# Kernel tuning notes

Measured on AMD Instinct MI355X. Metric: run time of the kernel, lower is better.

The kernel has to match this reference:

```python
import jax, jax.numpy as jnp
import numpy as np

PE_DIM = 64

def _layernorm(x, g, b, eps=1e-5):
    m = jnp.mean(x, -1, keepdims=True)
    v = jnp.mean((x - m) ** 2, -1, keepdims=True)
    return (x - m) * jax.lax.rsqrt(v + eps) * g + b

def _sinusoidal_pe(t, dim=PE_DIM):
    half = dim // 2
    freqs = jnp.exp(-jnp.log(10000.0) * jnp.arange(half) / half).astype(t.dtype)
    ang = t[..., None] * freqs  # [..., half]
    return jnp.concatenate([jnp.sin(ang), jnp.cos(ang)], -1)

def _bilinear(feats, b, t, x, y):
    # feats [B,Wl,H,W,D]; b,t int32 [B,Q,Wl,M] (b broadcastable); x,y in [0,1]
    # matches torch grid_sample(mode=bilinear, padding_mode=border, align_corners=False)
    H, W = feats.shape[2], feats.shape[3]
    px = x * W - 0.5
    py = y * H - 0.5
    x0 = jnp.floor(px); y0 = jnp.floor(py)
    wx = (px - x0)[..., None]; wy = (py - y0)[..., None]
    x0i = jnp.clip(x0.astype(jnp.int32), 0, W - 1)
    x1i = jnp.clip(x0.astype(jnp.int32) + 1, 0, W - 1)
    y0i = jnp.clip(y0.astype(jnp.int32), 0, H - 1)
    y1i = jnp.clip(y0.astype(jnp.int32) + 1, 0, H - 1)
    v00 = feats[b, t, y0i, x0i]  # [B,Q,Wl,M,D]
    v01 = feats[b, t, y0i, x1i]
    v10 = feats[b, t, y1i, x0i]
    v11 = feats[b, t, y1i, x1i]
    return (v00 * (1 - wy) * (1 - wx) + v01 * (1 - wy) * wx
            + v10 * wy * (1 - wx) + v11 * wy * wx)

def setup_inputs() -> dict:
    key = jax.random.key(0)
    ks = jax.random.split(key, 20)
    B, Q, Wl, H, W, D, M = 4, 300, 8, 64, 64, 256, 4
    s = 0.02
    inp = {
        'q': jax.random.normal(ks[0], (B, Q, D), jnp.float32),
        'kv_feats': jax.random.normal(ks[1], (B, Wl, H, W, D), jnp.float32),
        'kv_mask': jnp.zeros((B, Wl, H, W), jnp.bool_),
        'delta_sec': jax.random.normal(ks[2], (B, Q, Wl), jnp.float32),
        'w_ref': jax.random.normal(ks[3], (D, 2), jnp.float32) * s,
        'b_ref': jnp.zeros((2,), jnp.float32),
        'w_delta': jax.random.normal(ks[4], (2 * D, 3 * M), jnp.float32) * s,
        'b_delta': jnp.zeros((3 * M,), jnp.float32),
        'w_alpha': jax.random.normal(ks[5], (2 * D, M), jnp.float32) * s,
        'b_alpha': jnp.zeros((M,), jnp.float32),
        'lam': jnp.array(1.0, jnp.float32),
        'w_proj': jax.random.normal(ks[6], (D, D), jnp.float32) * s,
        'b_proj': jnp.zeros((D,), jnp.float32),
        'ln1_g': jnp.ones((D,), jnp.float32), 'ln1_b': jnp.zeros((D,), jnp.float32),
        'ln2_g': jnp.ones((D,), jnp.float32), 'ln2_b': jnp.zeros((D,), jnp.float32),
        'w_ffn1': jax.random.normal(ks[7], (D, 4 * D), jnp.float32) * s,
        'b_ffn1': jnp.zeros((4 * D,), jnp.float32),
        'w_ffn2': jax.random.normal(ks[8], (4 * D, D), jnp.float32) * s,
        'b_ffn2': jnp.zeros((D,), jnp.float32),
        'w_rel': jax.random.normal(ks[9], (PE_DIM, D), jnp.float32) * s,
        'b_rel': jnp.zeros((D,), jnp.float32),
    }
    return inp

def reference(q, kv_feats, kv_mask, delta_sec, w_ref, b_ref, w_delta, b_delta,
              w_alpha, b_alpha, lam, w_proj, b_proj, ln1_g, ln1_b, ln2_g, ln2_b,
              w_ffn1, b_ffn1, w_ffn2, b_ffn2, w_rel, b_rel):
    B, Q, D = q.shape
    Wl = kv_feats.shape[1]
    M = w_alpha.shape[1]

    qn = _layernorm(q, ln1_g, ln1_b)
    rel_feat = _sinusoidal_pe(delta_sec) @ w_rel + b_rel          # [B,Q,Wl,D]
    psi = jnp.concatenate([jnp.broadcast_to(qn[:, :, None, :], (B, Q, Wl, D)),
                           rel_feat], -1)                          # [B,Q,Wl,2D]

    delta = (psi @ w_delta + b_delta).reshape(B, Q, Wl, M, 3)
    logits = psi @ w_alpha + b_alpha                               # [B,Q,Wl,M]
    ref = jax.nn.sigmoid(qn @ w_ref + b_ref)                       # [B,Q,2]
    coords = ref[:, :, None, None, :] + jnp.tanh(delta[..., :2])   # [B,Q,Wl,M,2]
    coords = jnp.clip(coords, 0.0, 1.0)
    delta_t = jnp.tanh(delta[..., 2])                              # [B,Q,Wl,M]

    # mask features (mask==True -> invalid -> zero)
    feats = kv_feats * (~kv_mask)[..., None].astype(kv_feats.dtype)

    # temporal trilinear indices
    base = jnp.arange(Wl, dtype=q.dtype).reshape(1, 1, Wl, 1)
    target = base + delta_t
    t0f = jnp.clip(jnp.floor(target), 0, Wl - 1)
    t1f = jnp.clip(t0f + 1, 0, Wl - 1)
    alpha = (target - t0f)[..., None]
    t0 = t0f.astype(jnp.int32); t1 = t1f.astype(jnp.int32)

    bidx = jnp.arange(B, dtype=jnp.int32).reshape(B, 1, 1, 1)
    cx = coords[..., 0]; cy = coords[..., 1]
    s0 = _bilinear(feats, bidx, t0, cx, cy)                        # [B,Q,Wl,M,D]
    s1 = _bilinear(feats, bidx, t1, cx, cy)
    sampled = s0 * (1 - alpha) + s1 * alpha

    lam_sp = jax.nn.softplus(lam)
    weights = jax.nn.softmax(logits - lam_sp * jnp.abs(delta_sec)[..., None], axis=-1)
    agg = jnp.sum(weights[..., None] * sampled, axis=(2, 3))       # [B,Q,D]

    out = q + (agg @ w_proj + b_proj)
    h = _layernorm(out, ln2_g, ln2_b)
    ffn = jax.nn.gelu(h @ w_ffn1 + b_ffn1, approximate=False) @ w_ffn2 + b_ffn2
    return out + ffn
```

## Files before the change

### kernel.cpp

```cpp
#include <hip/hip_runtime.h>
#include <math.h>

#define Bn 4
#define Qn 300
#define WL 8
#define Hh 64
#define Ww 64
#define Dd 256
#define Mm 4

__device__ __forceinline__ float wave_reduce(float v) {
#pragma unroll
    for (int off = 32; off > 0; off >>= 1) v += __shfl_down(v, off, 64);
    return v;
}

__device__ __forceinline__ float block_reduce256(float v, float* lds) {
    v = wave_reduce(v);
    int lane = threadIdx.x & 63, wv = threadIdx.x >> 6;
    if (lane == 0) lds[wv] = v;
    __syncthreads();
    float r = lds[0] + lds[1] + lds[2] + lds[3];
    __syncthreads();
    return r;
}

__global__ void __launch_bounds__(256) k_pts(const float* __restrict__ q,
                                             const float* __restrict__ g1,
                                             const float* __restrict__ b1,
                                             const float* __restrict__ w_ref,
                                             const float* __restrict__ b_ref,
                                             const float* __restrict__ dsec,
                                             const float* __restrict__ w_rel,
                                             const float* __restrict__ b_rel,
                                             const float* __restrict__ w_delta,
                                             const float* __restrict__ b_delta,
                                             const float* __restrict__ w_alpha,
                                             const float* __restrict__ b_alpha,
                                             float* __restrict__ prm) {
    __shared__ float lds[4];
    __shared__ float sref[2];
    __shared__ float sqn[256];
    __shared__ float pe[8][64];
    __shared__ float rel[8][260];
    __shared__ float WcT[16 * 516];
    __shared__ float res[8][16];

    int bq = blockIdx.x, t = threadIdx.x;

    float x = q[bq * Dd + t];
    float m = block_reduce256(x, lds) * (1.f / Dd);
    float dx = x - m;
    float v = block_reduce256(dx * dx, lds) * (1.f / Dd);
    float y = dx * rsqrtf(v + 1e-5f) * g1[t] + b1[t];
    sqn[t] = y;

    float s0 = block_reduce256(y * w_ref[t * 2 + 0], lds);
    float s1 = block_reduce256(y * w_ref[t * 2 + 1], lds);
    if (t == 0) {
        sref[0] = 1.f / (1.f + expf(-(s0 + b_ref[0])));
        sref[1] = 1.f / (1.f + expf(-(s1 + b_ref[1])));
    }

    {
        int wl = t >> 5, i = t & 31;
        float f = expf(-logf(10000.f) * (float)i * (1.f / 32.f));
        float a = dsec[bq * WL + wl] * f;
        pe[wl][i] = sinf(a);
        pe[wl][i + 32] = cosf(a);
    }

    for (int u = t; u < 512 * 16; u += 256) {
        int k = u >> 4, jj = u & 15;
        float w = (jj < 12) ? w_delta[k * 12 + jj] : w_alpha[k * 4 + (jj - 12)];
        WcT[jj * 516 + k] = w;
    }

    float wr[64];
#pragma unroll
    for (int k = 0; k < 64; k++) wr[k] = w_rel[k * Dd + t];
    __syncthreads();

    float brl = b_rel[t];
    for (int wl = 0; wl < WL; wl++) {
        float r = brl;
#pragma unroll
        for (int k = 0; k < 64; k++) r += pe[wl][k] * wr[k];
        rel[wl][t] = r;
    }
    __syncthreads();

    if (t < 128) {
        int wl = t >> 4, jj = t & 15;
        const float4* wrow = (const float4*)&WcT[jj * 516];
        const float4* qrow = (const float4*)sqn;
        const float4* rrow = (const float4*)&rel[wl][0];
        float s = 0.f;
#pragma unroll 8
        for (int k4 = 0; k4 < 64; k4++) {
            float4 a = qrow[k4], w = wrow[k4];
            s += a.x * w.x + a.y * w.y + a.z * w.z + a.w * w.w;
        }
#pragma unroll 8
        for (int k4 = 0; k4 < 64; k4++) {
            float4 a = rrow[k4], w = wrow[64 + k4];
            s += a.x * w.x + a.y * w.y + a.z * w.z + a.w * w.w;
        }
        s += (jj < 12) ? b_delta[jj] : b_alpha[jj - 12];
        res[wl][jj] = s;
    }
    __syncthreads();

    if (t < 32) {
        int wl = t >> 2, mm = t & 3;
        float l0 = res[wl][12], l1 = res[wl][13], l2 = res[wl][14], l3 = res[wl][15];
        float mx = fmaxf(fmaxf(l0, l1), fmaxf(l2, l3));
        float inv = 1.f / (expf(l0 - mx) + expf(l1 - mx) + expf(l2 - mx) + expf(l3 - mx));
        float wgt = expf(res[wl][12 + mm] - mx) * inv;

        float cx = fminf(fmaxf(sref[0] + tanhf(res[wl][mm * 3 + 0]), 0.f), 1.f);
        float cy = fminf(fmaxf(sref[1] + tanhf(res[wl][mm * 3 + 1]), 0.f), 1.f);
        float tgt = (float)wl + tanhf(res[wl][mm * 3 + 2]);
        float t0f = fminf(fmaxf(floorf(tgt), 0.f), (float)(WL - 1));
        float t1f = fminf(t0f + 1.f, (float)(WL - 1));
        float alpha = tgt - t0f;
        float px = cx * (float)Ww - 0.5f, py = cy * (float)Hh - 0.5f;
        float fx = floorf(px), fy = floorf(py);
        float wx = px - fx, wy = py - fy;
        float x0 = fminf(fmaxf(fx, 0.f), (float)(Ww - 1));
        float x1 = fminf(fmaxf(fx + 1.f, 0.f), (float)(Ww - 1));
        float y0 = fminf(fmaxf(fy, 0.f), (float)(Hh - 1));
        float y1 = fminf(fmaxf(fy + 1.f, 0.f), (float)(Hh - 1));
        float* o = prm + (size_t)(bq * 32 + t) * 12;
        o[0] = wgt; o[1] = alpha; o[2] = wx; o[3] = wy;
        o[4] = t0f; o[5] = t1f; o[6] = x0; o[7] = x1; o[8] = y0; o[9] = y1;
        o[10] = 0.f; o[11] = 0.f;
    }
}

__global__ void __launch_bounds__(256) k_sample(const float* __restrict__ feats,
                                                const unsigned char* __restrict__ mask,
                                                const float* __restrict__ prm,
                                                float* __restrict__ agg) {
    __shared__ float P[32 * 12];
    __shared__ float part[4][256];
    int bq = blockIdx.x, t = threadIdx.x;
    int b = bq / Qn;
    int l = t & 63, j = t >> 6;
    for (int i = t; i < 32 * 12; i += 256) P[i] = prm[(size_t)bq * (32 * 12) + i];
    __syncthreads();
    const float4* f4 = (const float4*)feats;
    float4 acc = {0.f, 0.f, 0.f, 0.f};
#pragma unroll 2
    for (int p8 = 0; p8 < 8; p8++) {
        const float* pp = &P[(j * 8 + p8) * 12];
        float wgt = pp[0], alpha = pp[1], wx = pp[2], wy = pp[3];
        int t0 = (int)pp[4], t1 = (int)pp[5];
        int x0 = (int)pp[6], x1 = (int)pp[7];
        int y0 = (int)pp[8], y1 = (int)pp[9];
        float w00 = (1.f - wy) * (1.f - wx), w01 = (1.f - wy) * wx;
        float w10 = wy * (1.f - wx), w11 = wy * wx;
        float wt0 = wgt * (1.f - alpha), wt1 = wgt * alpha;
#pragma unroll
        for (int s = 0; s < 2; s++) {
            int tt = s ? t1 : t0;
            float wts = s ? wt1 : wt0;
            int base = (b * WL + tt) * Hh;
            int i00 = (base + y0) * Ww + x0;
            int i01 = (base + y0) * Ww + x1;
            int i10 = (base + y1) * Ww + x0;
            int i11 = (base + y1) * Ww + x1;
            float c00 = wts * w00 * (mask[i00] ? 0.f : 1.f);
            float c01 = wts * w01 * (mask[i01] ? 0.f : 1.f);
            float c10 = wts * w10 * (mask[i10] ? 0.f : 1.f);
            float c11 = wts * w11 * (mask[i11] ? 0.f : 1.f);
            float4 v00 = f4[(size_t)i00 * 64 + l];
            float4 v01 = f4[(size_t)i01 * 64 + l];
            float4 v10 = f4[(size_t)i10 * 64 + l];
            float4 v11 = f4[(size_t)i11 * 64 + l];
            acc.x += c00 * v00.x + c01 * v01.x + c10 * v10.x + c11 * v11.x;
            acc.y += c00 * v00.y + c01 * v01.y + c10 * v10.y + c11 * v11.y;
            acc.z += c00 * v00.z + c01 * v01.z + c10 * v10.z + c11 * v11.z;
            acc.w += c00 * v00.w + c01 * v01.w + c10 * v10.w + c11 * v11.w;
        }
    }
    ((float4*)&part[j][0])[l] = acc;
    __syncthreads();
    agg[(size_t)bq * Dd + t] = part[0][t] + part[1][t] + part[2][t] + part[3][t];
}

__global__ void __launch_bounds__(1024) k_out(const float* __restrict__ q,
                                              const float* __restrict__ agg,
                                              const float* __restrict__ w_proj,
                                              const float* __restrict__ b_proj,
                                              const float* __restrict__ g2,
                                              const float* __restrict__ b2,
                                              const float* __restrict__ w_ffn1,
                                              const float* __restrict__ b_ffn1,
                                              const float* __restrict__ w_ffn2,
                                              const float* __restrict__ b_ffn2,
                                              float* __restrict__ out) {
    __shared__ float sA[4][256];
    __shared__ float sO[4][256];
    __shared__ float sH[4][256];
    __shared__ float sF[4][1024];
    __shared__ float sP[4][4][256];
    __shared__ float red[4][4];
    int t = threadIdx.x;
    int c = t & 255, j = t >> 8;
    int row0 = blockIdx.x * 4;

    sA[j][c] = agg[(size_t)(row0 + j) * Dd + c];
    __syncthreads();

    {
        float a0 = 0, a1 = 0, a2 = 0, a3 = 0;
        const float4* ar0 = (const float4*)&sA[0][j * 64];
        const float4* ar1 = (const float4*)&sA[1][j * 64];
        const float4* ar2 = (const float4*)&sA[2][j * 64];
        const float4* ar3 = (const float4*)&sA[3][j * 64];
        for (int k4 = 0; k4 < 16; k4++) {
            int k = j * 64 + k4 * 4;
            float w0 = w_proj[(k + 0) * Dd + c];
            float w1 = w_proj[(k + 1) * Dd + c];
            float w2 = w_proj[(k + 2) * Dd + c];
            float w3 = w_proj[(k + 3) * Dd + c];
            float4 h0 = ar0[k4], h1 = ar1[k4], h2 = ar2[k4], h3 = ar3[k4];
            a0 += h0.x * w0 + h0.y * w1 + h0.z * w2 + h0.w * w3;
            a1 += h1.x * w0 + h1.y * w1 + h1.z * w2 + h1.w * w3;
            a2 += h2.x * w0 + h2.y * w1 + h2.z * w2 + h2.w * w3;
            a3 += h3.x * w0 + h3.y * w1 + h3.z * w2 + h3.w * w3;
        }
        sP[j][0][c] = a0; sP[j][1][c] = a1; sP[j][2][c] = a2; sP[j][3][c] = a3;
    }
    __syncthreads();

    float o = sP[0][j][c] + sP[1][j][c] + sP[2][j][c] + sP[3][j][c]
            + q[(size_t)(row0 + j) * Dd + c] + b_proj[c];
    sO[j][c] = o;
    int wg = (t >> 6) & 3, lane = t & 63;
    float s = wave_reduce(o);
    if (lane == 0) red[j][wg] = s;
    __syncthreads();
    float mean = (red[j][0] + red[j][1] + red[j][2] + red[j][3]) * (1.f / 256.f);
    float dx = o - mean;
    float s2 = wave_reduce(dx * dx);
    __syncthreads();
    if (lane == 0) red[j][wg] = s2;
    __syncthreads();
    float var = (red[j][0] + red[j][1] + red[j][2] + red[j][3]) * (1.f / 256.f);
    float h = dx * rsqrtf(var + 1e-5f) * g2[c] + b2[c];
    sH[j][c] = h;
    __syncthreads();

    {
        float f0 = 0, f1 = 0, f2 = 0, f3 = 0;
        const float4* h0p = (const float4*)&sH[0][0];
        const float4* h1p = (const float4*)&sH[1][0];
        const float4* h2p = (const float4*)&sH[2][0];
        const float4* h3p = (const float4*)&sH[3][0];
        for (int k4 = 0; k4 < 64; k4++) {
            int k = k4 * 4;
            float w0 = w_ffn1[(size_t)(k + 0) * 1024 + t];
            float w1 = w_ffn1[(size_t)(k + 1) * 1024 + t];
            float w2 = w_ffn1[(size_t)(k + 2) * 1024 + t];
            float w3 = w_ffn1[(size_t)(k + 3) * 1024 + t];
            float4 h0 = h0p[k4], h1 = h1p[k4], h2 = h2p[k4], h3 = h3p[k4];
            f0 += h0.x * w0 + h0.y * w1 + h0.z * w2 + h0.w * w3;
            f1 += h1.x * w0 + h1.y * w1 + h1.z * w2 + h1.w * w3;
            f2 += h2.x * w0 + h2.y * w1 + h2.z * w2 + h2.w * w3;
            f3 += h3.x * w0 + h3.y * w1 + h3.z * w2 + h3.w * w3;
        }
        float bf = b_ffn1[t];
        float v0 = f0 + bf, v1 = f1 + bf, v2 = f2 + bf, v3 = f3 + bf;
        sF[0][t] = 0.5f * v0 * (1.f + erff(v0 * 0.70710678118654752f));
        sF[1][t] = 0.5f * v1 * (1.f + erff(v1 * 0.70710678118654752f));
        sF[2][t] = 0.5f * v2 * (1.f + erff(v2 * 0.70710678118654752f));
        sF[3][t] = 0.5f * v3 * (1.f + erff(v3 * 0.70710678118654752f));
    }
    __syncthreads();

    {
        float a0 = 0, a1 = 0, a2 = 0, a3 = 0;
        const float4* f0p = (const float4*)&sF[0][j * 256];
        const float4* f1p = (const float4*)&sF[1][j * 256];
        const float4* f2p = (const float4*)&sF[2][j * 256];
        const float4* f3p = (const float4*)&sF[3][j * 256];
        for (int k4 = 0; k4 < 64; k4++) {
            int k = j * 256 + k4 * 4;
            float w0 = w_ffn2[(size_t)(k + 0) * Dd + c];
            float w1 = w_ffn2[(size_t)(k + 1) * Dd + c];
            float w2 = w_ffn2[(size_t)(k + 2) * Dd + c];
            float w3 = w_ffn2[(size_t)(k + 3) * Dd + c];
            float4 h0 = f0p[k4], h1 = f1p[k4], h2 = f2p[k4], h3 = f3p[k4];
            a0 += h0.x * w0 + h0.y * w1 + h0.z * w2 + h0.w * w3;
            a1 += h1.x * w0 + h1.y * w1 + h1.z * w2 + h1.w * w3;
            a2 += h2.x * w0 + h2.y * w1 + h2.z * w2 + h2.w * w3;
            a3 += h3.x * w0 + h3.y * w1 + h3.z * w2 + h3.w * w3;
        }
        sP[j][0][c] = a0; sP[j][1][c] = a1; sP[j][2][c] = a2; sP[j][3][c] = a3;
    }
    __syncthreads();

    float r2 = sP[0][j][c] + sP[1][j][c] + sP[2][j][c] + sP[3][j][c];
    out[(size_t)(row0 + j) * Dd + c] = sO[j][c] + r2 + b_ffn2[c];
}

extern "C" void kernel_launch(void* const* d_in, const int* in_sizes, int n_in,
                              void* d_out, int out_size, void* d_ws, size_t ws_size,
                              hipStream_t stream) {
    const float* q        = (const float*)d_in[0];
    const float* kv_feats = (const float*)d_in[1];
    const unsigned char* kv_mask = (const unsigned char*)d_in[2];
    const float* delta_sec= (const float*)d_in[3];
    const float* w_ref    = (const float*)d_in[4];
    const float* b_ref    = (const float*)d_in[5];
    const float* w_delta  = (const float*)d_in[6];
    const float* b_delta  = (const float*)d_in[7];
    const float* w_alpha  = (const float*)d_in[8];
    const float* b_alpha  = (const float*)d_in[9];
    const float* w_proj   = (const float*)d_in[11];
    const float* b_proj   = (const float*)d_in[12];
    const float* ln1_g    = (const float*)d_in[13];
    const float* ln1_b    = (const float*)d_in[14];
    const float* ln2_g    = (const float*)d_in[15];
    const float* ln2_b    = (const float*)d_in[16];
    const float* w_ffn1   = (const float*)d_in[17];
    const float* b_ffn1   = (const float*)d_in[18];
    const float* w_ffn2   = (const float*)d_in[19];
    const float* b_ffn2   = (const float*)d_in[20];
    const float* w_rel    = (const float*)d_in[21];
    const float* b_rel    = (const float*)d_in[22];
    float* out = (float*)d_out;

    float* ws  = (float*)d_ws;
    float* prm = ws;
    float* agg = ws + 460800;

    const int BQ = Bn * Qn;
    k_pts<<<dim3(BQ), dim3(256), 0, stream>>>(q, ln1_g, ln1_b, w_ref, b_ref, delta_sec,
                                              w_rel, b_rel, w_delta, b_delta,
                                              w_alpha, b_alpha, prm);
    k_sample<<<dim3(BQ), dim3(256), 0, stream>>>(kv_feats, kv_mask, prm, agg);
    k_out<<<dim3(BQ / 4), dim3(1024), 0, stream>>>(q, agg, w_proj, b_proj, ln2_g, ln2_b,
                                                   w_ffn1, b_ffn1, w_ffn2, b_ffn2, out);
}
```

Measured before the change: 347.7 us.

## Pack MLP weights to bf16, precompute gather records, rebalance output kernel

```diff
diff --git a/kernel.cpp b/kernel.cpp
--- a/kernel.cpp
+++ b/kernel.cpp
@@ -25,7 +25,33 @@
     return r;
 }
 
-__global__ void __launch_bounds__(256) k_pts(const float* __restrict__ q,
+__device__ __forceinline__ float lo16(unsigned u) { return __uint_as_float(u << 16); }
+__device__ __forceinline__ float hi16(unsigned u) { return __uint_as_float(u & 0xffff0000u); }
+
+__device__ __forceinline__ unsigned bfp(float a, float b) {
+    unsigned ua = __float_as_uint(a); ua = (ua + 0x7fffu + ((ua >> 16) & 1u)) >> 16;
+    unsigned ub = __float_as_uint(b); ub = (ub + 0x7fffu + ((ub >> 16) & 1u)) >> 16;
+    return ua | (ub << 16);
+}
+
+__global__ void __launch_bounds__(256) k_pack(const float* __restrict__ wp,
+                                              const float* __restrict__ wf1,
+                                              const float* __restrict__ wf2,
+                                              unsigned* __restrict__ pk) {
+    int i = blockIdx.x * 256 + threadIdx.x;
+    if (i < 32768) {
+        int kk = i >> 8, c = i & 255;
+        pk[i] = bfp(wp[(2 * kk) * 256 + c], wp[(2 * kk + 1) * 256 + c]);
+    } else if (i < 163840) {
+        int i2 = i - 32768; int kk = i2 >> 10, c = i2 & 1023;
+        pk[i] = bfp(wf1[(2 * kk) * 1024 + c], wf1[(2 * kk + 1) * 1024 + c]);
+    } else {
+        int i3 = i - 163840; int kk = i3 >> 8, c = i3 & 255;
+        pk[i] = bfp(wf2[(2 * kk) * 256 + c], wf2[(2 * kk + 1) * 256 + c]);
+    }
+}
+
+__global__ void __launch_bounds__(256) k_mid(const float* __restrict__ q,
                                              const float* __restrict__ g1,
                                              const float* __restrict__ b1,
                                              const float* __restrict__ w_ref,
@@ -37,7 +63,8 @@
                                              const float* __restrict__ b_delta,
                                              const float* __restrict__ w_alpha,
                                              const float* __restrict__ b_alpha,
-                                             float* __restrict__ prm) {
+                                             const unsigned char* __restrict__ mask,
+                                             unsigned* __restrict__ prm2) {
     __shared__ float lds[4];
     __shared__ float sref[2];
     __shared__ float sqn[256];
@@ -83,9 +110,14 @@
 
     float brl = b_rel[t];
     for (int wl = 0; wl < WL; wl++) {
+        const float4* p4 = (const float4*)&pe[wl][0];
         float r = brl;
 #pragma unroll
-        for (int k = 0; k < 64; k++) r += pe[wl][k] * wr[k];
+        for (int k4 = 0; k4 < 16; k4++) {
+            float4 p = p4[k4];
+            r += p.x * wr[4 * k4] + p.y * wr[4 * k4 + 1]
+               + p.z * wr[4 * k4 + 2] + p.w * wr[4 * k4 + 3];
+        }
         rel[wl][t] = r;
     }
     __syncthreads();
@@ -127,183 +159,220 @@
         float px = cx * (float)Ww - 0.5f, py = cy * (float)Hh - 0.5f;
         float fx = floorf(px), fy = floorf(py);
         float wx = px - fx, wy = py - fy;
-        float x0 = fminf(fmaxf(fx, 0.f), (float)(Ww - 1));
-        float x1 = fminf(fmaxf(fx + 1.f, 0.f), (float)(Ww - 1));
-        float y0 = fminf(fmaxf(fy, 0.f), (float)(Hh - 1));
-        float y1 = fminf(fmaxf(fy + 1.f, 0.f), (float)(Hh - 1));
-        float* o = prm + (size_t)(bq * 32 + t) * 12;
-        o[0] = wgt; o[1] = alpha; o[2] = wx; o[3] = wy;
-        o[4] = t0f; o[5] = t1f; o[6] = x0; o[7] = x1; o[8] = y0; o[9] = y1;
-        o[10] = 0.f; o[11] = 0.f;
-    }
-}
-
-__global__ void __launch_bounds__(256) k_sample(const float* __restrict__ feats,
-                                                const unsigned char* __restrict__ mask,
-                                                const float* __restrict__ prm,
-                                                float* __restrict__ agg) {
-    __shared__ float P[32 * 12];
-    __shared__ float part[4][256];
-    int bq = blockIdx.x, t = threadIdx.x;
-    int b = bq / Qn;
-    int l = t & 63, j = t >> 6;
-    for (int i = t; i < 32 * 12; i += 256) P[i] = prm[(size_t)bq * (32 * 12) + i];
-    __syncthreads();
-    const float4* f4 = (const float4*)feats;
-    float4 acc = {0.f, 0.f, 0.f, 0.f};
-#pragma unroll 2
-    for (int p8 = 0; p8 < 8; p8++) {
-        const float* pp = &P[(j * 8 + p8) * 12];
-        float wgt = pp[0], alpha = pp[1], wx = pp[2], wy = pp[3];
-        int t0 = (int)pp[4], t1 = (int)pp[5];
-        int x0 = (int)pp[6], x1 = (int)pp[7];
-        int y0 = (int)pp[8], y1 = (int)pp[9];
+        int X0 = (int)fminf(fmaxf(fx, 0.f), (float)(Ww - 1));
+        int X1 = (int)fminf(fmaxf(fx + 1.f, 0.f), (float)(Ww - 1));
+        int Y0 = (int)fminf(fmaxf(fy, 0.f), (float)(Hh - 1));
+        int Y1 = (int)fminf(fmaxf(fy + 1.f, 0.f), (float)(Hh - 1));
+        int T0 = (int)t0f, T1 = (int)t1f;
+
         float w00 = (1.f - wy) * (1.f - wx), w01 = (1.f - wy) * wx;
         float w10 = wy * (1.f - wx), w11 = wy * wx;
         float wt0 = wgt * (1.f - alpha), wt1 = wgt * alpha;
-#pragma unroll
-        for (int s = 0; s < 2; s++) {
-            int tt = s ? t1 : t0;
-            float wts = s ? wt1 : wt0;
-            int base = (b * WL + tt) * Hh;
-            int i00 = (base + y0) * Ww + x0;
-            int i01 = (base + y0) * Ww + x1;
-            int i10 = (base + y1) * Ww + x0;
-            int i11 = (base + y1) * Ww + x1;
-            float c00 = wts * w00 * (mask[i00] ? 0.f : 1.f);
-            float c01 = wts * w01 * (mask[i01] ? 0.f : 1.f);
-            float c10 = wts * w10 * (mask[i10] ? 0.f : 1.f);
-            float c11 = wts * w11 * (mask[i11] ? 0.f : 1.f);
-            float4 v00 = f4[(size_t)i00 * 64 + l];
-            float4 v01 = f4[(size_t)i01 * 64 + l];
-            float4 v10 = f4[(size_t)i10 * 64 + l];
-            float4 v11 = f4[(size_t)i11 * 64 + l];
-            acc.x += c00 * v00.x + c01 * v01.x + c10 * v10.x + c11 * v11.x;
-            acc.y += c00 * v00.y + c01 * v01.y + c10 * v10.y + c11 * v11.y;
-            acc.z += c00 * v00.z + c01 * v01.z + c10 * v10.z + c11 * v11.z;
-            acc.w += c00 * v00.w + c01 * v01.w + c10 * v10.w + c11 * v11.w;
+
+        int b = bq / Qn;
+        int base0 = (b * WL + T0) * Hh;
+        int base1 = (b * WL + T1) * Hh;
+        int i00 = (base0 + Y0) * Ww + X0, i01 = (base0 + Y0) * Ww + X1;
+        int i10 = (base0 + Y1) * Ww + X0, i11 = (base0 + Y1) * Ww + X1;
+        int j00 = (base1 + Y0) * Ww + X0, j01 = (base1 + Y0) * Ww + X1;
+        int j10 = (base1 + Y1) * Ww + X0, j11 = (base1 + Y1) * Ww + X1;
+
+        unsigned* rec = prm2 + (unsigned)(bq * 32 + t) * 16;
+        rec[0] = __float_as_uint(wt0 * w00 * (mask[i00] ? 0.f : 1.f));
+        rec[1] = __float_as_uint(wt0 * w01 * (mask[i01] ? 0.f : 1.f));
+        rec[2] = __float_as_uint(wt0 * w10 * (mask[i10] ? 0.f : 1.f));
+        rec[3] = __float_as_uint(wt0 * w11 * (mask[i11] ? 0.f : 1.f));
+        rec[4] = __float_as_uint(wt1 * w00 * (mask[j00] ? 0.f : 1.f));
+        rec[5] = __float_as_uint(wt1 * w01 * (mask[j01] ? 0.f : 1.f));
+        rec[6] = __float_as_uint(wt1 * w10 * (mask[j10] ? 0.f : 1.f));
+        rec[7] = __float_as_uint(wt1 * w11 * (mask[j11] ? 0.f : 1.f));
+        rec[8] = i00; rec[9] = i01; rec[10] = i10; rec[11] = i11;
+        rec[12] = j00; rec[13] = j01; rec[14] = j10; rec[15] = j11;
+    }
+}
+
+__global__ void __launch_bounds__(512) k_gather(const float* __restrict__ feats,
+                                                const unsigned* __restrict__ prm2,
+                                                float* __restrict__ agg) {
+    __shared__ unsigned P[32 * 16];
+    __shared__ float part[8][256];
+    int bq = blockIdx.x, t = threadIdx.x;
+    int l = t & 63, j = t >> 6;
+    P[t] = prm2[(unsigned)bq * 512 + t];
+    __syncthreads();
+    const float4* f4 = (const float4*)feats;
+    float4 acc = {0.f, 0.f, 0.f, 0.f};
+#pragma unroll
+    for (int p = 0; p < 4; p++) {
+        const unsigned* rec = &P[(j * 4 + p) * 16];
+#pragma unroll
+        for (int cn = 0; cn < 8; cn++) {
+            float w = __uint_as_float(rec[cn]);
+            size_t idx = rec[8 + cn];
+            float4 v = f4[idx * 64 + l];
+            acc.x += w * v.x; acc.y += w * v.y; acc.z += w * v.z; acc.w += w * v.w;
         }
     }
     ((float4*)&part[j][0])[l] = acc;
     __syncthreads();
-    agg[(size_t)bq * Dd + t] = part[0][t] + part[1][t] + part[2][t] + part[3][t];
+    if (t < 256) {
+        float s = part[0][t] + part[1][t] + part[2][t] + part[3][t]
+                + part[4][t] + part[5][t] + part[6][t] + part[7][t];
+        agg[(size_t)bq * Dd + t] = s;
+    }
+}
+
+template<int R>
+__device__ __forceinline__ void out_body(int row0,
+        const float* __restrict__ q, const float* __restrict__ agg,
+        const unsigned* __restrict__ pkP, const float* __restrict__ b_proj,
+        const float* __restrict__ g2, const float* __restrict__ b2,
+        const unsigned* __restrict__ pkF1, const float* __restrict__ b_ffn1,
+        const unsigned* __restrict__ pkF2, const float* __restrict__ b_ffn2,
+        float* __restrict__ out,
+        float* sA, float* sO, float* sH, float* sF, float* sP, float* sRed) {
+    int t = threadIdx.x;
+    int c = t & 255, j = t >> 8;
+
+    for (int u = t; u < 256 * R; u += 1024) {
+        int r = u >> 8, cc = u & 255;
+        sA[r * 256 + cc] = agg[(size_t)(row0 + r) * Dd + cc];
+    }
+    __syncthreads();
+
+    {
+        float acc[R];
+#pragma unroll
+        for (int r = 0; r < R; r++) acc[r] = 0.f;
+        const unsigned* wp = pkP + (j * 32) * 256 + c;
+#pragma unroll 4
+        for (int q4 = 0; q4 < 16; q4++) {
+            unsigned u0 = wp[(2 * q4) * 256];
+            unsigned u1 = wp[(2 * q4 + 1) * 256];
+            float w0 = lo16(u0), w1 = hi16(u0), w2 = lo16(u1), w3 = hi16(u1);
+#pragma unroll
+            for (int r = 0; r < R; r++) {
+                float4 a = ((const float4*)&sA[r * 256 + j * 64])[q4];
+                acc[r] += a.x * w0 + a.y * w1 + a.z * w2 + a.w * w3;
+            }
+        }
+#pragma unroll
+        for (int r = 0; r < R; r++) sP[(j * 5 + r) * 256 + c] = acc[r];
+    }
+    __syncthreads();
+
+    for (int u = t; u < 256 * R; u += 1024) {
+        int r = u >> 8, cc = u & 255;
+        float o = sP[(0 * 5 + r) * 256 + cc] + sP[(1 * 5 + r) * 256 + cc]
+                + sP[(2 * 5 + r) * 256 + cc] + sP[(3 * 5 + r) * 256 + cc]
+                + q[(size_t)(row0 + r) * Dd + cc] + b_proj[cc];
+        sO[r * 256 + cc] = o;
+    }
+    __syncthreads();
+
+    {
+        int wv = t >> 6, l = t & 63;
+        if (wv < R) {
+            float4 v = ((const float4*)&sO[wv * 256])[l];
+            float s = v.x + v.y + v.z + v.w;
+            s = __shfl(wave_reduce(s), 0, 64);
+            float mean = s * (1.f / 256.f);
+            float d0 = v.x - mean, d1 = v.y - mean, d2 = v.z - mean, d3 = v.w - mean;
+            float ss = d0 * d0 + d1 * d1 + d2 * d2 + d3 * d3;
+            ss = __shfl(wave_reduce(ss), 0, 64);
+            float rstd = rsqrtf(ss * (1.f / 256.f) + 1e-5f);
+            if (l == 0) { sRed[wv * 2] = mean; sRed[wv * 2 + 1] = rstd; }
+        }
+    }
+    __syncthreads();
+    for (int u = t; u < 256 * R; u += 1024) {
+        int r = u >> 8, cc = u & 255;
+        sH[r * 256 + cc] = (sO[r * 256 + cc] - sRed[r * 2]) * sRed[r * 2 + 1] * g2[cc] + b2[cc];
+    }
+    __syncthreads();
+
+    {
+        float f[R];
+#pragma unroll
+        for (int r = 0; r < R; r++) f[r] = 0.f;
+        const unsigned* wp = pkF1 + t;
+#pragma unroll 4
+        for (int q4 = 0; q4 < 64; q4++) {
+            unsigned u0 = wp[(2 * q4) * 1024];
+            unsigned u1 = wp[(2 * q4 + 1) * 1024];
+            float w0 = lo16(u0), w1 = hi16(u0), w2 = lo16(u1), w3 = hi16(u1);
+#pragma unroll
+            for (int r = 0; r < R; r++) {
+                float4 h = ((const float4*)&sH[r * 256])[q4];
+                f[r] += h.x * w0 + h.y * w1 + h.z * w2 + h.w * w3;
+            }
+        }
+        float bf = b_ffn1[t];
+#pragma unroll
+        for (int r = 0; r < R; r++) {
+            float xx = f[r] + bf;
+            sF[r * 1024 + t] = 0.5f * xx * (1.f + erff(xx * 0.70710678118654752f));
+        }
+    }
+    __syncthreads();
+
+    {
+        float acc[R];
+#pragma unroll
+        for (int r = 0; r < R; r++) acc[r] = 0.f;
+        const unsigned* wp = pkF2 + (j * 128) * 256 + c;
+#pragma unroll 4
+        for (int q4 = 0; q4 < 64; q4++) {
+            unsigned u0 = wp[(2 * q4) * 256];
+            unsigned u1 = wp[(2 * q4 + 1) * 256];
+            float w0 = lo16(u0), w1 = hi16(u0), w2 = lo16(u1), w3 = hi16(u1);
+#pragma unroll
+            for (int r = 0; r < R; r++) {
+                float4 h = ((const float4*)&sF[r * 1024 + j * 256])[q4];
+                acc[r] += h.x * w0 + h.y * w1 + h.z * w2 + h.w * w3;
+            }
+        }
+#pragma unroll
+        for (int r = 0; r < R; r++) sP[(j * 5 + r) * 256 + c] = acc[r];
+    }
+    __syncthreads();
+
+    for (int u = t; u < 256 * R; u += 1024) {
+        int r = u >> 8, cc = u & 255;
+        float s = sP[(0 * 5 + r) * 256 + cc] + sP[(1 * 5 + r) * 256 + cc]
+                + sP[(2 * 5 + r) * 256 + cc] + sP[(3 * 5 + r) * 256 + cc];
+        out[(size_t)(row0 + r) * Dd + cc] = sO[r * 256 + cc] + s + b_ffn2[cc];
+    }
 }
 
 __global__ void __launch_bounds__(1024) k_out(const float* __restrict__ q,
                                               const float* __restrict__ agg,
-                                              const float* __restrict__ w_proj,
+                                              const unsigned* __restrict__ pkP,
                                               const float* __restrict__ b_proj,
                                               const float* __restrict__ g2,
                                               const float* __restrict__ b2,
-                                              const float* __restrict__ w_ffn1,
+                                              const unsigned* __restrict__ pkF1,
                                               const float* __restrict__ b_ffn1,
-                                              const float* __restrict__ w_ffn2,
+                                              const unsigned* __restrict__ pkF2,
                                               const float* __restrict__ b_ffn2,
                                               float* __restrict__ out) {
-    __shared__ float sA[4][256];
-    __shared__ float sO[4][256];
-    __shared__ float sH[4][256];
-    __shared__ float sF[4][1024];
-    __shared__ float sP[4][4][256];
-    __shared__ float red[4][4];
-    int t = threadIdx.x;
-    int c = t & 255, j = t >> 8;
-    int row0 = blockIdx.x * 4;
-
-    sA[j][c] = agg[(size_t)(row0 + j) * Dd + c];
-    __syncthreads();
-
-    {
-        float a0 = 0, a1 = 0, a2 = 0, a3 = 0;
-        const float4* ar0 = (const float4*)&sA[0][j * 64];
-        const float4* ar1 = (const float4*)&sA[1][j * 64];
-        const float4* ar2 = (const float4*)&sA[2][j * 64];
-        const float4* ar3 = (const float4*)&sA[3][j * 64];
-        for (int k4 = 0; k4 < 16; k4++) {
-            int k = j * 64 + k4 * 4;
-            float w0 = w_proj[(k + 0) * Dd + c];
-            float w1 = w_proj[(k + 1) * Dd + c];
-            float w2 = w_proj[(k + 2) * Dd + c];
-            float w3 = w_proj[(k + 3) * Dd + c];
-            float4 h0 = ar0[k4], h1 = ar1[k4], h2 = ar2[k4], h3 = ar3[k4];
-            a0 += h0.x * w0 + h0.y * w1 + h0.z * w2 + h0.w * w3;
-            a1 += h1.x * w0 + h1.y * w1 + h1.z * w2 + h1.w * w3;
-            a2 += h2.x * w0 + h2.y * w1 + h2.z * w2 + h2.w * w3;
-            a3 += h3.x * w0 + h3.y * w1 + h3.z * w2 + h3.w * w3;
-        }
-        sP[j][0][c] = a0; sP[j][1][c] = a1; sP[j][2][c] = a2; sP[j][3][c] = a3;
-    }
-    __syncthreads();
-
-    float o = sP[0][j][c] + sP[1][j][c] + sP[2][j][c] + sP[3][j][c]
-            + q[(size_t)(row0 + j) * Dd + c] + b_proj[c];
-    sO[j][c] = o;
-    int wg = (t >> 6) & 3, lane = t & 63;
-    float s = wave_reduce(o);
-    if (lane == 0) red[j][wg] = s;
-    __syncthreads();
-    float mean = (red[j][0] + red[j][1] + red[j][2] + red[j][3]) * (1.f / 256.f);
-    float dx = o - mean;
-    float s2 = wave_reduce(dx * dx);
-    __syncthreads();
-    if (lane == 0) red[j][wg] = s2;
-    __syncthreads();
-    float var = (red[j][0] + red[j][1] + red[j][2] + red[j][3]) * (1.f / 256.f);
-    float h = dx * rsqrtf(var + 1e-5f) * g2[c] + b2[c];
-    sH[j][c] = h;
-    __syncthreads();
-
-    {
-        float f0 = 0, f1 = 0, f2 = 0, f3 = 0;
-        const float4* h0p = (const float4*)&sH[0][0];
-        const float4* h1p = (const float4*)&sH[1][0];
-        const float4* h2p = (const float4*)&sH[2][0];
-        const float4* h3p = (const float4*)&sH[3][0];
-        for (int k4 = 0; k4 < 64; k4++) {
-            int k = k4 * 4;
-            float w0 = w_ffn1[(size_t)(k + 0) * 1024 + t];
-            float w1 = w_ffn1[(size_t)(k + 1) * 1024 + t];
-            float w2 = w_ffn1[(size_t)(k + 2) * 1024 + t];
-            float w3 = w_ffn1[(size_t)(k + 3) * 1024 + t];
-            float4 h0 = h0p[k4], h1 = h1p[k4], h2 = h2p[k4], h3 = h3p[k4];
-            f0 += h0.x * w0 + h0.y * w1 + h0.z * w2 + h0.w * w3;
-            f1 += h1.x * w0 + h1.y * w1 + h1.z * w2 + h1.w * w3;
-            f2 += h2.x * w0 + h2.y * w1 + h2.z * w2 + h2.w * w3;
-            f3 += h3.x * w0 + h3.y * w1 + h3.z * w2 + h3.w * w3;
-        }
-        float bf = b_ffn1[t];
-        float v0 = f0 + bf, v1 = f1 + bf, v2 = f2 + bf, v3 = f3 + bf;
-        sF[0][t] = 0.5f * v0 * (1.f + erff(v0 * 0.70710678118654752f));
-        sF[1][t] = 0.5f * v1 * (1.f + erff(v1 * 0.70710678118654752f));
-        sF[2][t] = 0.5f * v2 * (1.f + erff(v2 * 0.70710678118654752f));
-        sF[3][t] = 0.5f * v3 * (1.f + erff(v3 * 0.70710678118654752f));
-    }
-    __syncthreads();
-
-    {
-        float a0 = 0, a1 = 0, a2 = 0, a3 = 0;
-        const float4* f0p = (const float4*)&sF[0][j * 256];
-        const float4* f1p = (const float4*)&sF[1][j * 256];
-        const float4* f2p = (const float4*)&sF[2][j * 256];
-        const float4* f3p = (const float4*)&sF[3][j * 256];
-        for (int k4 = 0; k4 < 64; k4++) {
-            int k = j * 256 + k4 * 4;
-            float w0 = w_ffn2[(size_t)(k + 0) * Dd + c];
-            float w1 = w_ffn2[(size_t)(k + 1) * Dd + c];
-            float w2 = w_ffn2[(size_t)(k + 2) * Dd + c];
-            float w3 = w_ffn2[(size_t)(k + 3) * Dd + c];
-            float4 h0 = f0p[k4], h1 = f1p[k4], h2 = f2p[k4], h3 = f3p[k4];
-            a0 += h0.x * w0 + h0.y * w1 + h0.z * w2 + h0.w * w3;
-            a1 += h1.x * w0 + h1.y * w1 + h1.z * w2 + h1.w * w3;
-            a2 += h2.x * w0 + h2.y * w1 + h2.z * w2 + h2.w * w3;
-            a3 += h3.x * w0 + h3.y * w1 + h3.z * w2 + h3.w * w3;
-        }
-        sP[j][0][c] = a0; sP[j][1][c] = a1; sP[j][2][c] = a2; sP[j][3][c] = a3;
-    }
-    __syncthreads();
-
-    float r2 = sP[0][j][c] + sP[1][j][c] + sP[2][j][c] + sP[3][j][c];
-    out[(size_t)(row0 + j) * Dd + c] = sO[j][c] + r2 + b_ffn2[c];
+    __shared__ float sA[5 * 256];
+    __shared__ float sO[5 * 256];
+    __shared__ float sH[5 * 256];
+    __shared__ float sF[5 * 1024];
+    __shared__ float sP[4 * 5 * 256];
+    __shared__ float sRed[16];
+    __shared__ float pad[8192];
+    if (b_ffn2 == nullptr) pad[threadIdx.x] = 0.f;
+
+    int bid = blockIdx.x;
+    if (bid < 176) {
+        out_body<5>(bid * 5, q, agg, pkP, b_proj, g2, b2, pkF1, b_ffn1, pkF2, b_ffn2,
+                    out, sA, sO, sH, sF, sP, sRed);
+    } else {
+        out_body<4>(880 + (bid - 176) * 4, q, agg, pkP, b_proj, g2, b2, pkF1, b_ffn1,
+                    pkF2, b_ffn2, out, sA, sO, sH, sF, sP, sRed);
+    }
 }
 
 extern "C" void kernel_launch(void* const* d_in, const int* in_sizes, int n_in,
@@ -333,15 +402,19 @@
     const float* b_rel    = (const float*)d_in[22];
     float* out = (float*)d_out;
 
-    float* ws  = (float*)d_ws;
-    float* prm = ws;
-    float* agg = ws + 460800;
+    unsigned* pk   = (unsigned*)d_ws;
+    unsigned* pkP  = pk;
+    unsigned* pkF1 = pk + 32768;
+    unsigned* pkF2 = pk + 163840;
+    unsigned* prm2 = pk + 294912;
+    float*    agg  = (float*)(pk + 294912 + 614400);
 
     const int BQ = Bn * Qn;
-    k_pts<<<dim3(BQ), dim3(256), 0, stream>>>(q, ln1_g, ln1_b, w_ref, b_ref, delta_sec,
+    k_pack<<<dim3(1152), dim3(256), 0, stream>>>(w_proj, w_ffn1, w_ffn2, pk);
+    k_mid<<<dim3(BQ), dim3(256), 0, stream>>>(q, ln1_g, ln1_b, w_ref, b_ref, delta_sec,
                                               w_rel, b_rel, w_delta, b_delta,
-                                              w_alpha, b_alpha, prm);
-    k_sample<<<dim3(BQ), dim3(256), 0, stream>>>(kv_feats, kv_mask, prm, agg);
-    k_out<<<dim3(BQ / 4), dim3(1024), 0, stream>>>(q, agg, w_proj, b_proj, ln2_g, ln2_b,
-                                                   w_ffn1, b_ffn1, w_ffn2, b_ffn2, out);
-}
+                                              w_alpha, b_alpha, kv_mask, prm2);
+    k_gather<<<dim3(BQ), dim3(512), 0, stream>>>(kv_feats, prm2, agg);
+    k_out<<<dim3(256), dim3(1024), 0, stream>>>(q, agg, pkP, b_proj, ln2_g, ln2_b,
+                                                pkF1, b_ffn1, pkF2, b_ffn2, out);
+}
```

Result: faster. 307.9 us (-11.4%).
